# Kernel tuning notes

Measured on AMD Instinct MI355X. Metric: run time of the kernel, lower is better.

The kernel has to match this reference:

```python
import jax, jax.numpy as jnp
import numpy as np

# Blade order: 1 | e0 e1 e2 e3 | e01 e02 e03 e12 e13 e23 | e012 e013 e023 e123 | e0123
GRADE = jnp.array([0, 1, 1, 1, 1, 2, 2, 2, 2, 2, 2, 3, 3, 3, 3, 4])
# Invariant bilinear form <~A B>_0 for signature (+,-,-,-)
METRIC = jnp.array([1., 1., -1., -1., -1., -1., -1., -1., 1., 1., 1., 1., 1., 1., -1., -1.], dtype=jnp.float32)
NUM_HEADS, HID_MV, HID_S = 8, 8, 32


def equi_linear(mv, s, w_mv, w_s2mv, w_mv2s, w_s, b_mv, b_s):
    """Pin(1,3)-equivariant linear layer: grade-projection basis maps + scalar<->grade-0 mixing."""
    w16 = w_mv[:, :, GRADE]  # (out_mv, in_mv, 16): one weight per grade, broadcast over blades
    out_mv = jnp.einsum('oix,...ix->...ox', w16, mv)
    out_mv = out_mv.at[..., 0].add(jnp.einsum('oi,...i->...o', w_s2mv, s) + b_mv)
    out_s = (jnp.einsum('oi,...i->...o', w_s, s)
             + jnp.einsum('oi,...i->...o', w_mv2s, mv[..., 0]) + b_s)
    return out_mv, out_s


def setup_inputs() -> dict:
    key = jax.random.key(0)
    ks = jax.random.split(key, 20)
    B, Nq, Nkv = 4, 2048, 2048
    H, Cm, Cs = NUM_HEADS, HID_MV, HID_S

    def w(k, shape, fan_in):
        return jax.random.normal(k, shape, jnp.float32) / np.sqrt(fan_in).astype(np.float32)

    return {
        'multivectors_kv': jax.random.normal(ks[0], (B, Nkv, 16, 16), jnp.float32),
        'multivectors_q': jax.random.normal(ks[1], (B, Nq, 16, 16), jnp.float32),
        'scalars_kv': jax.random.normal(ks[2], (B, Nkv, 64), jnp.float32),
        'scalars_q': jax.random.normal(ks[3], (B, Nq, 64), jnp.float32),
        # q_linear: 16 mv -> Cm*H=64 mv, 64 s -> Cs*H=256 s
        'wq_mv': w(ks[4], (Cm * H, 16, 5), 16), 'wq_s2mv': w(ks[5], (Cm * H, 64), 64),
        'wq_mv2s': w(ks[6], (Cs * H, 16), 16), 'wq_s': w(ks[7], (Cs * H, 64), 64),
        'bq_mv': jnp.zeros((Cm * H,), jnp.float32), 'bq_s': jnp.zeros((Cs * H,), jnp.float32),
        # kv_linear: 16 mv -> 2*Cm=16 mv, 64 s -> 2*Cs=64 s (multi-query: shared across heads)
        'wkv_mv': w(ks[8], (2 * Cm, 16, 5), 16), 'wkv_s2mv': w(ks[9], (2 * Cm, 64), 64),
        'wkv_mv2s': w(ks[10], (2 * Cs, 16), 16), 'wkv_s': w(ks[11], (2 * Cs, 64), 64),
        'bkv_mv': jnp.zeros((2 * Cm,), jnp.float32), 'bkv_s': jnp.zeros((2 * Cs,), jnp.float32),
        # out_linear: Cm*H=64 mv -> 16 mv, Cs*H=256 s -> 64 s
        'wo_mv': w(ks[12], (16, Cm * H, 5), Cm * H), 'wo_s2mv': w(ks[13], (16, Cs * H), Cs * H),
        'wo_mv2s': w(ks[14], (64, Cm * H), Cm * H), 'wo_s': w(ks[15], (64, Cs * H), Cs * H),
        'bo_mv': jnp.zeros((16,), jnp.float32), 'bo_s': jnp.zeros((64,), jnp.float32),
        'head_scale': jnp.ones((H,), jnp.float32),
    }


def reference(multivectors_kv, multivectors_q, scalars_kv, scalars_q,
              wq_mv, wq_s2mv, wq_mv2s, wq_s, bq_mv, bq_s,
              wkv_mv, wkv_s2mv, wkv_mv2s, wkv_s, bkv_mv, bkv_s,
              wo_mv, wo_s2mv, wo_mv2s, wo_s, bo_mv, bo_s, head_scale):
    B, Nq = multivectors_q.shape[0], multivectors_q.shape[1]
    H, Cm, Cs = NUM_HEADS, HID_MV, HID_S

    q_mv, q_s = equi_linear(multivectors_q, scalars_q, wq_mv, wq_s2mv, wq_mv2s, wq_s, bq_mv, bq_s)
    kv_mv, kv_s = equi_linear(multivectors_kv, scalars_kv, wkv_mv, wkv_s2mv, wkv_mv2s, wkv_s, bkv_mv, bkv_s)
    k_mv, v_mv = jnp.split(kv_mv, 2, axis=-2)  # (B,Nkv,Cm,16) each
    k_s, v_s = jnp.split(kv_s, 2, axis=-1)     # (B,Nkv,Cs) each

    # einops '(hidden num_heads)': hidden is the outer factor
    q_mv = jnp.moveaxis(q_mv.reshape(B, Nq, Cm, H, 16), 3, 1)  # (B,H,Nq,Cm,16)
    q_s = jnp.moveaxis(q_s.reshape(B, Nq, Cs, H), 3, 1)        # (B,H,Nq,Cs)

    scale = np.float32(1.0 / np.sqrt(16 * Cm + Cs))  # flattened feature dim
    scores = (jnp.einsum('bhqcx,bkcx->bhqk', q_mv, k_mv * METRIC)
              + jnp.einsum('bhqs,bks->bhqk', q_s, k_s)) * scale
    attn = jax.nn.softmax(scores, axis=-1)  # (B,H,Nq,Nkv)
    h_mv = jnp.einsum('bhqk,bkcx->bhqcx', attn, v_mv)
    h_s = jnp.einsum('bhqk,bks->bhqs', attn, v_s)

    h_mv = h_mv * head_scale[None, :, None, None, None]
    h_s = h_s * head_scale[None, :, None, None]

    # '(n_heads hidden_channels)': heads outer
    h_mv = jnp.moveaxis(h_mv, 1, 2).reshape(B, Nq, H * Cm, 16)
    h_s = jnp.moveaxis(h_s, 1, 2).reshape(B, Nq, H * Cs)

    return equi_linear(h_mv, h_s, wo_mv, wo_s2mv, wo_mv2s, wo_s, bo_mv, bo_s)
```

## Files before the change

### kernel.cpp

```cpp
#include <hip/hip_runtime.h>
#include <hip/hip_bf16.h>
#include <cstdint>

#define H_  8
#define B_  4
#define NQ  2048
#define NKV 2048
#define DF  160

typedef __attribute__((ext_vector_type(8))) short bf16x8;
typedef __attribute__((ext_vector_type(4))) float f32x4;

__constant__ int   c_grade[16]  = {0,1,1,1,1,2,2,2,2,2,2,3,3,3,3,4};
__constant__ float c_metric[16] = {1.f,1.f,-1.f,-1.f,-1.f,-1.f,-1.f,-1.f,
                                   1.f,1.f,1.f,1.f,1.f,1.f,-1.f,-1.f};

#define SCALE_LOG2E 0.11405506f

__device__ __forceinline__ unsigned short f2bf(float f) {
    union { float f; unsigned u; } v; v.f = f;
    return (unsigned short)((v.u + 0x7FFFu + ((v.u >> 16) & 1u)) >> 16);
}
__device__ __forceinline__ float bf2f(unsigned short u) {
    union { unsigned u; float f; } v; v.u = ((unsigned)u) << 16;
    return v.f;
}

__global__ __launch_bounds__(256) void qproj_kernel(
    const float* __restrict__ mvq,
    const float* __restrict__ sq,
    const float* __restrict__ w_mv,
    const float* __restrict__ w_s2mv,
    const float* __restrict__ w_mv2s,
    const float* __restrict__ w_s,
    const float* __restrict__ b_mv,
    const float* __restrict__ b_s,
    unsigned short* __restrict__ Qbuf)
{
    const int tok0 = blockIdx.x * 16;
    const int b = tok0 / NQ, n0 = tok0 % NQ;
    const int t = threadIdx.x;

    __shared__ float mv_t[256][20];
    __shared__ float s_t[64][20];
    __shared__ float smadd[64][20];

    #pragma unroll
    for (int k = 0; k < 16; ++k)
        mv_t[t][k] = mvq[(size_t)(tok0 + k) * 256 + t];
    {
        int e = t & 63, tb = t >> 6;
        #pragma unroll
        for (int k = 0; k < 4; ++k)
            s_t[e][tb + 4 * k] = sq[(size_t)(tok0 + tb + 4 * k) * 64 + e];
    }
    __syncthreads();

    {
        int o = t >> 2, tg = t & 3;
        f32x4 acc = {0.f, 0.f, 0.f, 0.f};
        for (int i = 0; i < 64; ++i)
            acc += w_s2mv[o * 64 + i] * *(const f32x4*)&s_t[i][tg * 4];
        acc += b_mv[o];
        *(f32x4*)&smadd[o][tg * 4] = acc;
    }
    __syncthreads();

    const int x = t & 15;
    const int g = c_grade[x];
    const int obase = t >> 4;
    {
        float wreg[4][16];
        #pragma unroll
        for (int p = 0; p < 4; ++p) {
            int o = obase + 16 * p;
            #pragma unroll
            for (int i = 0; i < 16; ++i)
                wreg[p][i] = w_mv[(o * 16 + i) * 5 + g];
        }
        #pragma unroll
        for (int k = 0; k < 4; ++k) {
            f32x4 rows[16];
            #pragma unroll
            for (int i = 0; i < 16; ++i)
                rows[i] = *(const f32x4*)&mv_t[i * 16 + x][k * 4];
            #pragma unroll
            for (int p = 0; p < 4; ++p) {
                int o = obase + 16 * p;
                f32x4 acc = {0.f, 0.f, 0.f, 0.f};
                #pragma unroll
                for (int i = 0; i < 16; ++i)
                    acc += wreg[p][i] * rows[i];
                if (x == 0) acc += *(const f32x4*)&smadd[o][k * 4];
                int c = o >> 3, h = o & 7;
                #pragma unroll
                for (int j = 0; j < 4; ++j)
                    Qbuf[((size_t)(b * H_ + h) * NQ + n0 + k * 4 + j) * DF + c * 16 + x] =
                        f2bf(acc[j] * SCALE_LOG2E);
            }
        }
    }

    {
        f32x4 acc[4] = {{0,0,0,0},{0,0,0,0},{0,0,0,0},{0,0,0,0}};
        const float4* ws4 = (const float4*)w_s;
        #pragma unroll
        for (int ii = 0; ii < 16; ++ii) {
            float4 w4 = ws4[t * 16 + ii];
            #pragma unroll
            for (int c = 0; c < 4; ++c) {
                float w = (&w4.x)[c];
                #pragma unroll
                for (int k = 0; k < 4; ++k)
                    acc[k] += w * *(const f32x4*)&s_t[ii * 4 + c][k * 4];
            }
        }
        #pragma unroll
        for (int i = 0; i < 16; ++i) {
            float w = w_mv2s[t * 16 + i];
            #pragma unroll
            for (int k = 0; k < 4; ++k)
                acc[k] += w * *(const f32x4*)&mv_t[i * 16][k * 4];
        }
        float bs = b_s[t];
        int cs = t >> 3, h = t & 7;
        #pragma unroll
        for (int k = 0; k < 4; ++k)
            #pragma unroll
            for (int j = 0; j < 4; ++j)
                Qbuf[((size_t)(b * H_ + h) * NQ + n0 + k * 4 + j) * DF + 128 + cs] =
                    f2bf((acc[k][j] + bs) * SCALE_LOG2E);
    }
}

__global__ __launch_bounds__(256) void kvproj_kernel(
    const float* __restrict__ mvkv, const float* __restrict__ skv,
    const float* __restrict__ w_mv,
    const float* __restrict__ w_s2mv,
    const float* __restrict__ w_mv2s,
    const float* __restrict__ w_s,
    const float* __restrict__ b_mv,
    const float* __restrict__ b_s,
    unsigned short* __restrict__ Kbuf,
    unsigned short* __restrict__ Vtbuf)
{
    const int tok0 = blockIdx.x * 16;
    const int b = tok0 / NKV, n0 = tok0 % NKV;
    const int t = threadIdx.x;

    __shared__ float mv_t[256][20];
    __shared__ float s_t[64][20];
    __shared__ float smadd[16][20];

    #pragma unroll
    for (int k = 0; k < 16; ++k)
        mv_t[t][k] = mvkv[(size_t)(tok0 + k) * 256 + t];
    {
        int e = t & 63, tb = t >> 6;
        #pragma unroll
        for (int k = 0; k < 4; ++k)
            s_t[e][tb + 4 * k] = skv[(size_t)(tok0 + tb + 4 * k) * 64 + e];
    }
    __syncthreads();

    {
        int o = t >> 4, tau = t & 15;
        float acc = 0.f;
        for (int i = 0; i < 64; ++i)
            acc += w_s2mv[o * 64 + i] * s_t[i][tau];
        smadd[o][tau] = acc + b_mv[o];
    }
    __syncthreads();

    {
        int o = t >> 4, x = t & 15, g = c_grade[x];
        f32x4 acc[4] = {{0,0,0,0},{0,0,0,0},{0,0,0,0},{0,0,0,0}};
        #pragma unroll
        for (int i = 0; i < 16; ++i) {
            float w = w_mv[(o * 16 + i) * 5 + g];
            #pragma unroll
            for (int k = 0; k < 4; ++k)
                acc[k] += w * *(const f32x4*)&mv_t[i * 16 + x][k * 4];
        }
        if (x == 0) {
            #pragma unroll
            for (int k = 0; k < 4; ++k)
                acc[k] += *(const f32x4*)&smadd[o][k * 4];
        }
        if (o < 8) {
            float met = c_metric[x];
            #pragma unroll
            for (int k = 0; k < 4; ++k)
                #pragma unroll
                for (int j = 0; j < 4; ++j)
                    Kbuf[((size_t)b * NKV + n0 + k * 4 + j) * DF + o * 16 + x] =
                        f2bf(acc[k][j] * met);
        } else {
            uint4 pk[2];
            unsigned* pu = (unsigned*)&pk[0];
            #pragma unroll
            for (int q = 0; q < 8; ++q) {
                int k = q >> 1, j = (q & 1) * 2;
                pu[q] = (unsigned)f2bf(acc[k][j]) | ((unsigned)f2bf(acc[k][j + 1]) << 16);
            }
            unsigned short* dst = Vtbuf + ((size_t)b * DF + (o - 8) * 16 + x) * NKV + n0;
            ((uint4*)dst)[0] = pk[0];
            ((uint4*)dst)[1] = pk[1];
        }
    }

    {
        int o2 = t & 63, tg = t >> 6;
        f32x4 acc = {0.f, 0.f, 0.f, 0.f};
        const float4* ws4 = (const float4*)w_s;
        #pragma unroll
        for (int ii = 0; ii < 16; ++ii) {
            float4 w4 = ws4[o2 * 16 + ii];
            #pragma unroll
            for (int c = 0; c < 4; ++c)
                acc += (&w4.x)[c] * *(const f32x4*)&s_t[ii * 4 + c][tg * 4];
        }
        #pragma unroll
        for (int i = 0; i < 16; ++i)
            acc += w_mv2s[o2 * 16 + i] * *(const f32x4*)&mv_t[i * 16][tg * 4];
        acc += b_s[o2];
        if (o2 < 32) {
            #pragma unroll
            for (int j = 0; j < 4; ++j)
                Kbuf[((size_t)b * NKV + n0 + tg * 4 + j) * DF + 128 + o2] = f2bf(acc[j]);
        } else {
            uint2 pk;
            pk.x = (unsigned)f2bf(acc[0]) | ((unsigned)f2bf(acc[1]) << 16);
            pk.y = (unsigned)f2bf(acc[2]) | ((unsigned)f2bf(acc[3]) << 16);
            *(uint2*)(Vtbuf + ((size_t)b * DF + 128 + o2 - 32) * NKV + n0 + tg * 4) = pk;
        }
    }
}

__global__ __launch_bounds__(256, 2) void attn_kernel(
    const unsigned short* __restrict__ Qb,
    const unsigned short* __restrict__ Kb0,
    const unsigned short* __restrict__ Vb0,
    const float* __restrict__ head_scale,
    unsigned short* __restrict__ Hb)
{
    const int qt = blockIdx.x, hp = blockIdx.y, b = blockIdx.z;
    const int tid  = threadIdx.x;
    const int w    = tid >> 6;
    const int lane = tid & 63;
    const int l16  = lane & 15;
    const int lq   = lane >> 4;
    const int qbase = qt * 64;

    __shared__ __align__(16) unsigned short Ksh[64][168];
    __shared__ __align__(16) unsigned short Vsh[160][72];
    __shared__ __align__(16) unsigned short Psh[2][4][16][72];

    bf16x8 onesf;
    #pragma unroll
    for (int j = 0; j < 8; ++j) onesf[j] = (short)0x3F80;

    bf16x8 qf[2][5];
    #pragma unroll
    for (int s = 0; s < 2; ++s) {
        const unsigned short* qrow =
            Qb + ((size_t)(b * H_ + hp * 2 + s) * NQ + qbase + w * 16 + l16) * DF;
        #pragma unroll
        for (int ks = 0; ks < 5; ++ks)
            qf[s][ks] = *reinterpret_cast<const bf16x8*>(qrow + ks * 32 + lq * 8);
    }

    f32x4 O[2][11];
    #pragma unroll
    for (int s = 0; s < 2; ++s)
        #pragma unroll
        for (int d = 0; d < 11; ++d) O[s][d] = f32x4{0.f, 0.f, 0.f, 0.f};

    const unsigned short* Kb = Kb0 + (size_t)b * NKV * DF;
    const unsigned short* Vb = Vb0 + (size_t)b * DF * NKV;

    for (int kt = 0; kt < NKV / 64; ++kt) {
        __syncthreads();
        #pragma unroll
        for (int c = 0; c < 5; ++c) {
            int idx = tid + c * 256;
            int r = idx / 20, col = idx % 20;
            *reinterpret_cast<uint4*>(&Ksh[r][col * 8]) =
                *reinterpret_cast<const uint4*>(Kb + (size_t)(kt * 64 + r) * DF + col * 8);
        }
        #pragma unroll
        for (int c = 0; c < 5; ++c) {
            int idx = tid + c * 256;
            int r = idx >> 3, col = idx & 7;
            *reinterpret_cast<uint4*>(&Vsh[r][col * 8]) =
                *reinterpret_cast<const uint4*>(Vb + (size_t)r * NKV + kt * 64 + col * 8);
        }
        __syncthreads();

        f32x4 sc[2][4];
        #pragma unroll
        for (int nt = 0; nt < 4; ++nt) {
            sc[0][nt] = f32x4{0.f, 0.f, 0.f, 0.f};
            sc[1][nt] = f32x4{0.f, 0.f, 0.f, 0.f};
            #pragma unroll
            for (int ks = 0; ks < 5; ++ks) {
                bf16x8 kf = *reinterpret_cast<const bf16x8*>(
                    &Ksh[nt * 16 + l16][ks * 32 + lq * 8]);
                sc[0][nt] = __builtin_amdgcn_mfma_f32_16x16x32_bf16(qf[0][ks], kf, sc[0][nt], 0, 0, 0);
                sc[1][nt] = __builtin_amdgcn_mfma_f32_16x16x32_bf16(qf[1][ks], kf, sc[1][nt], 0, 0, 0);
            }
        }

        #pragma unroll
        for (int s = 0; s < 2; ++s)
            #pragma unroll
            for (int nt = 0; nt < 4; ++nt)
                #pragma unroll
                for (int r = 0; r < 4; ++r)
                    Psh[s][w][lq * 4 + r][nt * 16 + l16] =
                        f2bf(__builtin_amdgcn_exp2f(sc[s][nt][r]));

        #pragma unroll
        for (int k2 = 0; k2 < 2; ++k2) {
            bf16x8 pf0 = *reinterpret_cast<const bf16x8*>(&Psh[0][w][l16][k2 * 32 + lq * 8]);
            bf16x8 pf1 = *reinterpret_cast<const bf16x8*>(&Psh[1][w][l16][k2 * 32 + lq * 8]);
            O[0][10] = __builtin_amdgcn_mfma_f32_16x16x32_bf16(pf0, onesf, O[0][10], 0, 0, 0);
            O[1][10] = __builtin_amdgcn_mfma_f32_16x16x32_bf16(pf1, onesf, O[1][10], 0, 0, 0);
            #pragma unroll
            for (int d = 0; d < 10; ++d) {
                bf16x8 vf = *reinterpret_cast<const bf16x8*>(
                    &Vsh[d * 16 + l16][k2 * 32 + lq * 8]);
                O[0][d] = __builtin_amdgcn_mfma_f32_16x16x32_bf16(pf0, vf, O[0][d], 0, 0, 0);
                O[1][d] = __builtin_amdgcn_mfma_f32_16x16x32_bf16(pf1, vf, O[1][d], 0, 0, 0);
            }
        }
    }

    #pragma unroll
    for (int s = 0; s < 2; ++s) {
        float hsc = head_scale[hp * 2 + s];
        #pragma unroll
        for (int r = 0; r < 4; ++r) {
            float inv = hsc / O[s][10][r];
            int qrow = qbase + w * 16 + lq * 4 + r;
            unsigned short* orow =
                Hb + ((size_t)(b * H_ + hp * 2 + s) * NQ + qrow) * DF;
            #pragma unroll
            for (int d = 0; d < 10; ++d)
                orow[d * 16 + l16] = f2bf(O[s][d][r] * inv);
        }
    }
}

__global__ __launch_bounds__(256) void oproj_kernel(
    const unsigned short* __restrict__ Hb,
    const float* __restrict__ w_mv,
    const float* __restrict__ w_s2mv,
    const float* __restrict__ w_mv2s,
    const float* __restrict__ w_s,
    const float* __restrict__ b_mv,
    const float* __restrict__ b_s,
    float* __restrict__ out)
{
    const int tok0 = blockIdx.x * 8;
    const int b = tok0 / NQ, n0 = tok0 % NQ;
    const int t = threadIdx.x;

    __shared__ float hmv_t[1024][12];
    __shared__ float hs_t[256][12];
    __shared__ float s2v[16][8];

    #pragma unroll
    for (int hh = 0; hh < 8; ++hh) {
        #pragma unroll
        for (int j = 0; j < 5; ++j) {
            int flat = t + 256 * j;
            int tau = flat / 160, d = flat % 160;
            float v = bf2f(Hb[((size_t)(b * H_ + hh) * NQ + n0 + tau) * DF + d]);
            if (d < 128) hmv_t[hh * 128 + d][tau] = v;
            else         hs_t[hh * 32 + d - 128][tau] = v;
        }
    }
    __syncthreads();

    {
        int o2 = t >> 4, tau = (t >> 1) & 7, ih = t & 1;
        float acc = 0.f;
        for (int ii = 0; ii < 128; ++ii) {
            int i = ih * 128 + ii;
            acc += w_s2mv[o2 * 256 + i] * hs_t[i][tau];
        }
        acc += __shfl_xor(acc, 1);
        if (ih == 0) s2v[o2][tau] = acc + b_mv[o2];
    }
    __syncthreads();

    {
        int o2 = t >> 4, x = t & 15, g = c_grade[x];
        f32x4 a0 = {0,0,0,0}, a1 = {0,0,0,0};
        for (int i = 0; i < 64; ++i) {
            float w = w_mv[(o2 * 64 + i) * 5 + g];
            a0 += w * *(const f32x4*)&hmv_t[i * 16 + x][0];
            a1 += w * *(const f32x4*)&hmv_t[i * 16 + x][4];
        }
        if (x == 0) {
            a0 += *(const f32x4*)&s2v[o2][0];
            a1 += *(const f32x4*)&s2v[o2][4];
        }
        #pragma unroll
        for (int j = 0; j < 4; ++j) {
            out[(size_t)(tok0 + j) * 256 + o2 * 16 + x] = a0[j];
            out[(size_t)(tok0 + 4 + j) * 256 + o2 * 16 + x] = a1[j];
        }
    }

    {
        int o2 = t & 63, th = t >> 6;
        float a0 = b_s[o2], a1 = b_s[o2];
        const float4* ws4 = (const float4*)w_s;
        for (int ii = 0; ii < 64; ++ii) {
            float4 w4 = ws4[o2 * 64 + ii];
            #pragma unroll
            for (int c = 0; c < 4; ++c) {
                int i = ii * 4 + c;
                float w = (&w4.x)[c];
                a0 += w * hs_t[i][th * 2];
                a1 += w * hs_t[i][th * 2 + 1];
            }
        }
        for (int i = 0; i < 64; ++i) {
            float w = w_mv2s[o2 * 64 + i];
            a0 += w * hmv_t[i * 16][th * 2];
            a1 += w * hmv_t[i * 16][th * 2 + 1];
        }
        size_t sbase = (size_t)B_ * NQ * 256;
        out[sbase + (size_t)(tok0 + th * 2) * 64 + o2] = a0;
        out[sbase + (size_t)(tok0 + th * 2 + 1) * 64 + o2] = a1;
    }
}

extern "C" void kernel_launch(void* const* d_in, const int* in_sizes, int n_in,
                              void* d_out, int out_size, void* d_ws, size_t ws_size,
                              hipStream_t stream) {
    const float* mv_kv  = (const float*)d_in[0];
    const float* mv_q   = (const float*)d_in[1];
    const float* s_kv   = (const float*)d_in[2];
    const float* s_q    = (const float*)d_in[3];
    const float* wq_mv  = (const float*)d_in[4];
    const float* wq_s2mv= (const float*)d_in[5];
    const float* wq_mv2s= (const float*)d_in[6];
    const float* wq_s   = (const float*)d_in[7];
    const float* bq_mv  = (const float*)d_in[8];
    const float* bq_s   = (const float*)d_in[9];
    const float* wkv_mv = (const float*)d_in[10];
    const float* wkv_s2mv=(const float*)d_in[11];
    const float* wkv_mv2s=(const float*)d_in[12];
    const float* wkv_s  = (const float*)d_in[13];
    const float* bkv_mv = (const float*)d_in[14];
    const float* bkv_s  = (const float*)d_in[15];
    const float* wo_mv  = (const float*)d_in[16];
    const float* wo_s2mv= (const float*)d_in[17];
    const float* wo_mv2s= (const float*)d_in[18];
    const float* wo_s   = (const float*)d_in[19];
    const float* bo_mv  = (const float*)d_in[20];
    const float* bo_s   = (const float*)d_in[21];
    const float* head_scale = (const float*)d_in[22];

    char* ws = (char*)d_ws;
    unsigned short* Qbuf  = (unsigned short*)(ws);
    unsigned short* Kbuf  = (unsigned short*)(ws + 20971520);
    unsigned short* Vtbuf = (unsigned short*)(ws + 23592960);
    unsigned short* Hbuf  = (unsigned short*)(ws + 26214400);

    qproj_kernel<<<B_ * NQ / 16, 256, 0, stream>>>(
        mv_q, s_q, wq_mv, wq_s2mv, wq_mv2s, wq_s, bq_mv, bq_s, Qbuf);
    kvproj_kernel<<<B_ * NKV / 16, 256, 0, stream>>>(
        mv_kv, s_kv, wkv_mv, wkv_s2mv, wkv_mv2s, wkv_s, bkv_mv, bkv_s, Kbuf, Vtbuf);
    dim3 g3(NQ / 64, H_ / 2, B_);
    attn_kernel<<<g3, 256, 0, stream>>>(Qbuf, Kbuf, Vtbuf, head_scale, Hbuf);
    oproj_kernel<<<B_ * NQ / 8, 256, 0, stream>>>(
        Hbuf, wo_mv, wo_s2mv, wo_mv2s, wo_s, bo_mv, bo_s, (float*)d_out);
}
```

Measured before the change: 290.4 us.

## Recast equivariant projections as dense bf16 MFMA GEMMs with expanded weights

Replaces the scalar-FMA q/kv/out projection kernels with weight-expansion kernels, which build dense bf16 matrices folding in grade broadcast, scalar mixing, bias (via a constant-one input column), metric and softmax scale. These are then consumed by MFMA-based GEMM kernels. The aim is to move the projection arithmetic onto matrix cores and cut FP32 VALU work. The cost is three extra launches per call to expand the weights, many zero-padded FLOPs, and inputs rounded to bf16 before the projections.

Result: slower. 332.2 us (+14.4%).

```diff
diff --git a/kernel.cpp b/kernel.cpp
--- a/kernel.cpp
+++ b/kernel.cpp
@@ -21,218 +21,315 @@
     union { float f; unsigned u; } v; v.f = f;
     return (unsigned short)((v.u + 0x7FFFu + ((v.u >> 16) & 1u)) >> 16);
 }
-__device__ __forceinline__ float bf2f(unsigned short u) {
-    union { unsigned u; float f; } v; v.u = ((unsigned)u) << 16;
-    return v.f;
-}
-
-__global__ __launch_bounds__(256) void qproj_kernel(
-    const float* __restrict__ mvq,
-    const float* __restrict__ sq,
-    const float* __restrict__ w_mv,
-    const float* __restrict__ w_s2mv,
-    const float* __restrict__ w_mv2s,
-    const float* __restrict__ w_s,
-    const float* __restrict__ b_mv,
-    const float* __restrict__ b_s,
-    unsigned short* __restrict__ Qbuf)
-{
-    const int tok0 = blockIdx.x * 16;
+
+__global__ __launch_bounds__(256) void expand_wq(
+    const float* __restrict__ wmv, const float* __restrict__ ws2mv,
+    const float* __restrict__ wmv2s, const float* __restrict__ ws,
+    const float* __restrict__ bmv, const float* __restrict__ bs,
+    unsigned short* __restrict__ Wq)
+{
+    const int j = blockIdx.x;
+    const int h = j / 160, pos = j % 160;
+    for (int k = threadIdx.x; k < 352; k += 256) {
+        float val = 0.f;
+        if (pos < 128) {
+            int c = pos >> 4, x = pos & 15, o = c * 8 + h, g = c_grade[x];
+            if (k < 256)       { if ((k & 15) == x) val = wmv[(o*16 + (k>>4))*5 + g]; }
+            else if (k < 320)  { if (x == 0) val = ws2mv[o*64 + (k-256)]; }
+            else if (k == 320) { if (x == 0) val = bmv[o]; }
+        } else {
+            int cs = pos - 128, o2 = cs * 8 + h;
+            if (k < 256)       { if ((k & 15) == 0) val = wmv2s[o2*16 + (k>>4)]; }
+            else if (k < 320)  val = ws[o2*64 + (k-256)];
+            else if (k == 320) val = bs[o2];
+        }
+        Wq[(size_t)j*352 + k] = f2bf(val * SCALE_LOG2E);
+    }
+}
+
+__global__ __launch_bounds__(256) void expand_wkv(
+    const float* __restrict__ wmv, const float* __restrict__ ws2mv,
+    const float* __restrict__ wmv2s, const float* __restrict__ ws,
+    const float* __restrict__ bmv, const float* __restrict__ bs,
+    unsigned short* __restrict__ Wkv)
+{
+    const int j = blockIdx.x;
+    const int side = j / 160, pos = j % 160;
+    for (int k = threadIdx.x; k < 352; k += 256) {
+        float val = 0.f, mult = 1.f;
+        if (pos < 128) {
+            int c = pos >> 4, x = pos & 15, o = side * 8 + c, g = c_grade[x];
+            if (side == 0) mult = c_metric[x];
+            if (k < 256)       { if ((k & 15) == x) val = wmv[(o*16 + (k>>4))*5 + g]; }
+            else if (k < 320)  { if (x == 0) val = ws2mv[o*64 + (k-256)]; }
+            else if (k == 320) { if (x == 0) val = bmv[o]; }
+        } else {
+            int s = pos - 128, o2 = side * 32 + s;
+            if (k < 256)       { if ((k & 15) == 0) val = wmv2s[o2*16 + (k>>4)]; }
+            else if (k < 320)  val = ws[o2*64 + (k-256)];
+            else if (k == 320) val = bs[o2];
+        }
+        Wkv[(size_t)j*352 + k] = f2bf(val * mult);
+    }
+}
+
+__global__ __launch_bounds__(256) void expand_wo(
+    const float* __restrict__ wmv, const float* __restrict__ ws2mv,
+    const float* __restrict__ wmv2s, const float* __restrict__ ws,
+    const float* __restrict__ bmv, const float* __restrict__ bs,
+    unsigned short* __restrict__ Wo)
+{
+    const int j = blockIdx.x;
+    for (int k = threadIdx.x; k < 1408; k += 256) {
+        float val = 0.f;
+        if (j < 256) {
+            int o2 = j >> 4, x = j & 15, g = c_grade[x];
+            if (k < 1280) {
+                int hh = k / 160, pp = k % 160;
+                if (pp < 128) { if ((pp & 15) == x) val = wmv[(o2*64 + hh*8 + (pp>>4))*5 + g]; }
+                else          { if (x == 0) val = ws2mv[o2*256 + hh*32 + (pp-128)]; }
+            } else if (k == 1280) { if (x == 0) val = bmv[o2]; }
+        } else {
+            int o2 = j - 256;
+            if (k < 1280) {
+                int hh = k / 160, pp = k % 160;
+                if (pp < 128) { if ((pp & 15) == 0) val = wmv2s[o2*64 + hh*8 + (pp>>4)]; }
+                else          val = ws[o2*256 + hh*32 + (pp-128)];
+            } else if (k == 1280) val = bs[o2];
+        }
+        Wo[(size_t)j*1408 + k] = f2bf(val);
+    }
+}
+
+#define ASTR 360
+#define WSTR 40
+
+__global__ __launch_bounds__(256) void gemm_q(
+    const float* __restrict__ mvq, const float* __restrict__ sq,
+    const unsigned short* __restrict__ Wq, unsigned short* __restrict__ Qbuf)
+{
+    const int tok0 = blockIdx.x * 64, h = blockIdx.y;
     const int b = tok0 / NQ, n0 = tok0 % NQ;
-    const int t = threadIdx.x;
-
-    __shared__ float mv_t[256][20];
-    __shared__ float s_t[64][20];
-    __shared__ float smadd[64][20];
-
-    #pragma unroll
-    for (int k = 0; k < 16; ++k)
-        mv_t[t][k] = mvq[(size_t)(tok0 + k) * 256 + t];
-    {
-        int e = t & 63, tb = t >> 6;
-        #pragma unroll
-        for (int k = 0; k < 4; ++k)
-            s_t[e][tb + 4 * k] = sq[(size_t)(tok0 + tb + 4 * k) * 64 + e];
+    const int t = threadIdx.x, w = t >> 6, lane = t & 63, l16 = lane & 15, lq = lane >> 4;
+
+    __shared__ __align__(16) unsigned short Ash[64][ASTR];
+    __shared__ __align__(16) unsigned short Wsh[160][WSTR];
+
+    const float4* mv4 = (const float4*)(mvq + (size_t)tok0 * 256);
+    const float4* s4  = (const float4*)(sq  + (size_t)tok0 * 64);
+    #pragma unroll
+    for (int r = 0; r < 20; ++r) {
+        int slot = t + 256 * r;
+        int tok = slot / 80, q = slot % 80;
+        float4 v = (q < 64) ? mv4[tok * 64 + q] : s4[tok * 16 + (q - 64)];
+        int col = (q < 64) ? q * 4 : 256 + (q - 64) * 4;
+        unsigned lo = (unsigned)f2bf(v.x) | ((unsigned)f2bf(v.y) << 16);
+        unsigned hi = (unsigned)f2bf(v.z) | ((unsigned)f2bf(v.w) << 16);
+        uint2 u; u.x = lo; u.y = hi;
+        *(uint2*)&Ash[tok][col] = u;
+    }
+    #pragma unroll
+    for (int r = 0; r < 9; ++r) {
+        int idx = t + 256 * r;
+        int tok = idx / 36, cc = idx % 36;
+        Ash[tok][320 + cc] = (cc == 0) ? (unsigned short)0x3F80 : (unsigned short)0;
     }
     __syncthreads();
 
-    {
-        int o = t >> 2, tg = t & 3;
-        f32x4 acc = {0.f, 0.f, 0.f, 0.f};
-        for (int i = 0; i < 64; ++i)
-            acc += w_s2mv[o * 64 + i] * *(const f32x4*)&s_t[i][tg * 4];
-        acc += b_mv[o];
-        *(f32x4*)&smadd[o][tg * 4] = acc;
+    bf16x8 af[11];
+    #pragma unroll
+    for (int ks = 0; ks < 11; ++ks)
+        af[ks] = *(const bf16x8*)&Ash[w * 16 + l16][ks * 32 + lq * 8];
+
+    f32x4 acc[10];
+    #pragma unroll
+    for (int nt = 0; nt < 10; ++nt) acc[nt] = f32x4{0.f, 0.f, 0.f, 0.f};
+
+    const unsigned short* Wbase = Wq + (size_t)h * 160 * 352;
+    for (int ks = 0; ks < 11; ++ks) {
+        __syncthreads();
+        #pragma unroll
+        for (int r = 0; r < 3; ++r) {
+            int s = t + 256 * r;
+            if (s < 640) {
+                int row = s >> 2, c4 = s & 3;
+                *(uint4*)&Wsh[row][c4 * 8] =
+                    *(const uint4*)(Wbase + (size_t)row * 352 + ks * 32 + c4 * 8);
+            }
+        }
+        __syncthreads();
+        #pragma unroll
+        for (int nt = 0; nt < 10; ++nt) {
+            bf16x8 wf = *(const bf16x8*)&Wsh[nt * 16 + l16][lq * 8];
+            acc[nt] = __builtin_amdgcn_mfma_f32_16x16x32_bf16(af[ks], wf, acc[nt], 0, 0, 0);
+        }
+    }
+
+    unsigned short* qb = Qbuf + ((size_t)(b * H_ + h) * NQ + n0) * DF;
+    #pragma unroll
+    for (int nt = 0; nt < 10; ++nt)
+        #pragma unroll
+        for (int r = 0; r < 4; ++r) {
+            int tok = w * 16 + 4 * lq + r;
+            qb[(size_t)tok * DF + nt * 16 + l16] = f2bf(acc[nt][r]);
+        }
+}
+
+__global__ __launch_bounds__(256) void gemm_kv(
+    const float* __restrict__ mvkv, const float* __restrict__ skv,
+    const unsigned short* __restrict__ Wkv,
+    unsigned short* __restrict__ Kbuf, unsigned short* __restrict__ Vtbuf)
+{
+    const int tok0 = blockIdx.x * 64, slice = blockIdx.y;
+    const int b = tok0 / NKV, n0 = tok0 % NKV;
+    const int t = threadIdx.x, w = t >> 6, lane = t & 63, l16 = lane & 15, lq = lane >> 4;
+
+    __shared__ __align__(16) unsigned short Ash[64][ASTR];
+    __shared__ __align__(16) unsigned short Wsh[160][WSTR];
+
+    const float4* mv4 = (const float4*)(mvkv + (size_t)tok0 * 256);
+    const float4* s4  = (const float4*)(skv  + (size_t)tok0 * 64);
+    #pragma unroll
+    for (int r = 0; r < 20; ++r) {
+        int slot = t + 256 * r;
+        int tok = slot / 80, q = slot % 80;
+        float4 v = (q < 64) ? mv4[tok * 64 + q] : s4[tok * 16 + (q - 64)];
+        int col = (q < 64) ? q * 4 : 256 + (q - 64) * 4;
+        unsigned lo = (unsigned)f2bf(v.x) | ((unsigned)f2bf(v.y) << 16);
+        unsigned hi = (unsigned)f2bf(v.z) | ((unsigned)f2bf(v.w) << 16);
+        uint2 u; u.x = lo; u.y = hi;
+        *(uint2*)&Ash[tok][col] = u;
+    }
+    #pragma unroll
+    for (int r = 0; r < 9; ++r) {
+        int idx = t + 256 * r;
+        int tok = idx / 36, cc = idx % 36;
+        Ash[tok][320 + cc] = (cc == 0) ? (unsigned short)0x3F80 : (unsigned short)0;
     }
     __syncthreads();
 
-    const int x = t & 15;
-    const int g = c_grade[x];
-    const int obase = t >> 4;
-    {
-        float wreg[4][16];
-        #pragma unroll
-        for (int p = 0; p < 4; ++p) {
-            int o = obase + 16 * p;
-            #pragma unroll
-            for (int i = 0; i < 16; ++i)
-                wreg[p][i] = w_mv[(o * 16 + i) * 5 + g];
-        }
-        #pragma unroll
-        for (int k = 0; k < 4; ++k) {
-            f32x4 rows[16];
-            #pragma unroll
-            for (int i = 0; i < 16; ++i)
-                rows[i] = *(const f32x4*)&mv_t[i * 16 + x][k * 4];
-            #pragma unroll
-            for (int p = 0; p < 4; ++p) {
-                int o = obase + 16 * p;
-                f32x4 acc = {0.f, 0.f, 0.f, 0.f};
-                #pragma unroll
-                for (int i = 0; i < 16; ++i)
-                    acc += wreg[p][i] * rows[i];
-                if (x == 0) acc += *(const f32x4*)&smadd[o][k * 4];
-                int c = o >> 3, h = o & 7;
-                #pragma unroll
-                for (int j = 0; j < 4; ++j)
-                    Qbuf[((size_t)(b * H_ + h) * NQ + n0 + k * 4 + j) * DF + c * 16 + x] =
-                        f2bf(acc[j] * SCALE_LOG2E);
-            }
-        }
-    }
-
-    {
-        f32x4 acc[4] = {{0,0,0,0},{0,0,0,0},{0,0,0,0},{0,0,0,0}};
-        const float4* ws4 = (const float4*)w_s;
-        #pragma unroll
-        for (int ii = 0; ii < 16; ++ii) {
-            float4 w4 = ws4[t * 16 + ii];
-            #pragma unroll
-            for (int c = 0; c < 4; ++c) {
-                float w = (&w4.x)[c];
-                #pragma unroll
-                for (int k = 0; k < 4; ++k)
-                    acc[k] += w * *(const f32x4*)&s_t[ii * 4 + c][k * 4];
-            }
-        }
-        #pragma unroll
-        for (int i = 0; i < 16; ++i) {
-            float w = w_mv2s[t * 16 + i];
-            #pragma unroll
-            for (int k = 0; k < 4; ++k)
-                acc[k] += w * *(const f32x4*)&mv_t[i * 16][k * 4];
-        }
-        float bs = b_s[t];
-        int cs = t >> 3, h = t & 7;
-        #pragma unroll
-        for (int k = 0; k < 4; ++k)
-            #pragma unroll
-            for (int j = 0; j < 4; ++j)
-                Qbuf[((size_t)(b * H_ + h) * NQ + n0 + k * 4 + j) * DF + 128 + cs] =
-                    f2bf((acc[k][j] + bs) * SCALE_LOG2E);
-    }
-}
-
-__global__ __launch_bounds__(256) void kvproj_kernel(
-    const float* __restrict__ mvkv, const float* __restrict__ skv,
-    const float* __restrict__ w_mv,
-    const float* __restrict__ w_s2mv,
-    const float* __restrict__ w_mv2s,
-    const float* __restrict__ w_s,
-    const float* __restrict__ b_mv,
-    const float* __restrict__ b_s,
-    unsigned short* __restrict__ Kbuf,
-    unsigned short* __restrict__ Vtbuf)
-{
-    const int tok0 = blockIdx.x * 16;
-    const int b = tok0 / NKV, n0 = tok0 % NKV;
-    const int t = threadIdx.x;
-
-    __shared__ float mv_t[256][20];
-    __shared__ float s_t[64][20];
-    __shared__ float smadd[16][20];
-
-    #pragma unroll
-    for (int k = 0; k < 16; ++k)
-        mv_t[t][k] = mvkv[(size_t)(tok0 + k) * 256 + t];
-    {
-        int e = t & 63, tb = t >> 6;
-        #pragma unroll
-        for (int k = 0; k < 4; ++k)
-            s_t[e][tb + 4 * k] = skv[(size_t)(tok0 + tb + 4 * k) * 64 + e];
-    }
-    __syncthreads();
-
-    {
-        int o = t >> 4, tau = t & 15;
-        float acc = 0.f;
-        for (int i = 0; i < 64; ++i)
-            acc += w_s2mv[o * 64 + i] * s_t[i][tau];
-        smadd[o][tau] = acc + b_mv[o];
-    }
-    __syncthreads();
-
-    {
-        int o = t >> 4, x = t & 15, g = c_grade[x];
-        f32x4 acc[4] = {{0,0,0,0},{0,0,0,0},{0,0,0,0},{0,0,0,0}};
-        #pragma unroll
-        for (int i = 0; i < 16; ++i) {
-            float w = w_mv[(o * 16 + i) * 5 + g];
-            #pragma unroll
-            for (int k = 0; k < 4; ++k)
-                acc[k] += w * *(const f32x4*)&mv_t[i * 16 + x][k * 4];
-        }
-        if (x == 0) {
-            #pragma unroll
-            for (int k = 0; k < 4; ++k)
-                acc[k] += *(const f32x4*)&smadd[o][k * 4];
-        }
-        if (o < 8) {
-            float met = c_metric[x];
-            #pragma unroll
-            for (int k = 0; k < 4; ++k)
-                #pragma unroll
-                for (int j = 0; j < 4; ++j)
-                    Kbuf[((size_t)b * NKV + n0 + k * 4 + j) * DF + o * 16 + x] =
-                        f2bf(acc[k][j] * met);
-        } else {
-            uint4 pk[2];
-            unsigned* pu = (unsigned*)&pk[0];
-            #pragma unroll
-            for (int q = 0; q < 8; ++q) {
-                int k = q >> 1, j = (q & 1) * 2;
-                pu[q] = (unsigned)f2bf(acc[k][j]) | ((unsigned)f2bf(acc[k][j + 1]) << 16);
-            }
-            unsigned short* dst = Vtbuf + ((size_t)b * DF + (o - 8) * 16 + x) * NKV + n0;
-            ((uint4*)dst)[0] = pk[0];
-            ((uint4*)dst)[1] = pk[1];
-        }
-    }
-
-    {
-        int o2 = t & 63, tg = t >> 6;
-        f32x4 acc = {0.f, 0.f, 0.f, 0.f};
-        const float4* ws4 = (const float4*)w_s;
-        #pragma unroll
-        for (int ii = 0; ii < 16; ++ii) {
-            float4 w4 = ws4[o2 * 16 + ii];
-            #pragma unroll
-            for (int c = 0; c < 4; ++c)
-                acc += (&w4.x)[c] * *(const f32x4*)&s_t[ii * 4 + c][tg * 4];
-        }
-        #pragma unroll
-        for (int i = 0; i < 16; ++i)
-            acc += w_mv2s[o2 * 16 + i] * *(const f32x4*)&mv_t[i * 16][tg * 4];
-        acc += b_s[o2];
-        if (o2 < 32) {
-            #pragma unroll
-            for (int j = 0; j < 4; ++j)
-                Kbuf[((size_t)b * NKV + n0 + tg * 4 + j) * DF + 128 + o2] = f2bf(acc[j]);
-        } else {
-            uint2 pk;
-            pk.x = (unsigned)f2bf(acc[0]) | ((unsigned)f2bf(acc[1]) << 16);
-            pk.y = (unsigned)f2bf(acc[2]) | ((unsigned)f2bf(acc[3]) << 16);
-            *(uint2*)(Vtbuf + ((size_t)b * DF + 128 + o2 - 32) * NKV + n0 + tg * 4) = pk;
+    bf16x8 af[11];
+    #pragma unroll
+    for (int ks = 0; ks < 11; ++ks)
+        af[ks] = *(const bf16x8*)&Ash[w * 16 + l16][ks * 32 + lq * 8];
+
+    f32x4 acc[10];
+    #pragma unroll
+    for (int nt = 0; nt < 10; ++nt) acc[nt] = f32x4{0.f, 0.f, 0.f, 0.f};
+
+    const unsigned short* Wbase = Wkv + (size_t)slice * 160 * 352;
+    for (int ks = 0; ks < 11; ++ks) {
+        __syncthreads();
+        #pragma unroll
+        for (int r = 0; r < 3; ++r) {
+            int s = t + 256 * r;
+            if (s < 640) {
+                int row = s >> 2, c4 = s & 3;
+                *(uint4*)&Wsh[row][c4 * 8] =
+                    *(const uint4*)(Wbase + (size_t)row * 352 + ks * 32 + c4 * 8);
+            }
+        }
+        __syncthreads();
+        #pragma unroll
+        for (int nt = 0; nt < 10; ++nt) {
+            bf16x8 wf = *(const bf16x8*)&Wsh[nt * 16 + l16][lq * 8];
+            acc[nt] = __builtin_amdgcn_mfma_f32_16x16x32_bf16(af[ks], wf, acc[nt], 0, 0, 0);
+        }
+    }
+
+    if (slice == 0) {
+        unsigned short* kb = Kbuf + ((size_t)b * NKV + n0) * DF;
+        #pragma unroll
+        for (int nt = 0; nt < 10; ++nt)
+            #pragma unroll
+            for (int r = 0; r < 4; ++r) {
+                int tok = w * 16 + 4 * lq + r;
+                kb[(size_t)tok * DF + nt * 16 + l16] = f2bf(acc[nt][r]);
+            }
+    } else {
+        unsigned short* vb = Vtbuf + (size_t)b * DF * NKV;
+        #pragma unroll
+        for (int nt = 0; nt < 10; ++nt) {
+            int pos = nt * 16 + l16;
+            unsigned lo = (unsigned)f2bf(acc[nt][0]) | ((unsigned)f2bf(acc[nt][1]) << 16);
+            unsigned hi = (unsigned)f2bf(acc[nt][2]) | ((unsigned)f2bf(acc[nt][3]) << 16);
+            uint2 u; u.x = lo; u.y = hi;
+            *(uint2*)(vb + (size_t)pos * NKV + n0 + w * 16 + 4 * lq) = u;
+        }
+    }
+}
+
+__global__ __launch_bounds__(256) void gemm_o(
+    const unsigned short* __restrict__ Hb, const unsigned short* __restrict__ Wo,
+    float* __restrict__ out)
+{
+    const int tok0 = blockIdx.x * 64, slice = blockIdx.y;
+    const int b = tok0 / NQ, n0 = tok0 % NQ;
+    const int t = threadIdx.x, w = t >> 6, lane = t & 63, l16 = lane & 15, lq = lane >> 4;
+
+    __shared__ __align__(16) unsigned short Ash[64][ASTR];
+    __shared__ __align__(16) unsigned short Wsh[160][WSTR];
+
+    f32x4 acc[10];
+    #pragma unroll
+    for (int nt = 0; nt < 10; ++nt) acc[nt] = f32x4{0.f, 0.f, 0.f, 0.f};
+
+    const unsigned short* Wbase = Wo + (size_t)slice * 160 * 1408;
+
+    for (int kc = 0; kc < 4; ++kc) {
+        __syncthreads();
+        #pragma unroll
+        for (int r = 0; r < 11; ++r) {
+            int s = t + 256 * r;
+            int tok = s / 44, g = s % 44;
+            int f0 = kc * 352 + g * 8;
+            uint4 val;
+            if (f0 < 1280) {
+                int hh = f0 / 160, pp = f0 % 160;
+                val = *(const uint4*)(Hb + ((size_t)(b * H_ + hh) * NQ + n0 + tok) * DF + pp);
+            } else if (f0 == 1280) {
+                val.x = 0x3F80u; val.y = 0; val.z = 0; val.w = 0;
+            } else {
+                val.x = 0; val.y = 0; val.z = 0; val.w = 0;
+            }
+            *(uint4*)&Ash[tok][g * 8] = val;
+        }
+        __syncthreads();
+
+        bf16x8 af[11];
+        #pragma unroll
+        for (int ks = 0; ks < 11; ++ks)
+            af[ks] = *(const bf16x8*)&Ash[w * 16 + l16][ks * 32 + lq * 8];
+
+        for (int ks = 0; ks < 11; ++ks) {
+            __syncthreads();
+            #pragma unroll
+            for (int r = 0; r < 3; ++r) {
+                int s = t + 256 * r;
+                if (s < 640) {
+                    int row = s >> 2, c4 = s & 3;
+                    *(uint4*)&Wsh[row][c4 * 8] =
+                        *(const uint4*)(Wbase + (size_t)row * 1408 + kc * 352 + ks * 32 + c4 * 8);
+                }
+            }
+            __syncthreads();
+            #pragma unroll
+            for (int nt = 0; nt < 10; ++nt) {
+                bf16x8 wf = *(const bf16x8*)&Wsh[nt * 16 + l16][lq * 8];
+                acc[nt] = __builtin_amdgcn_mfma_f32_16x16x32_bf16(af[ks], wf, acc[nt], 0, 0, 0);
+            }
+        }
+    }
+
+    const size_t sbase = (size_t)B_ * NQ * 256;
+    #pragma unroll
+    for (int nt = 0; nt < 10; ++nt) {
+        int j = slice * 160 + nt * 16 + l16;
+        #pragma unroll
+        for (int r = 0; r < 4; ++r) {
+            size_t tok = tok0 + w * 16 + 4 * lq + r;
+            if (j < 256) out[tok * 256 + j] = acc[nt][r];
+            else         out[sbase + tok * 64 + (j - 256)] = acc[nt][r];
         }
     }
 }
@@ -349,93 +446,6 @@
             for (int d = 0; d < 10; ++d)
                 orow[d * 16 + l16] = f2bf(O[s][d][r] * inv);
         }
-    }
-}
-
-__global__ __launch_bounds__(256) void oproj_kernel(
-    const unsigned short* __restrict__ Hb,
-    const float* __restrict__ w_mv,
-    const float* __restrict__ w_s2mv,
-    const float* __restrict__ w_mv2s,
-    const float* __restrict__ w_s,
-    const float* __restrict__ b_mv,
-    const float* __restrict__ b_s,
-    float* __restrict__ out)
-{
-    const int tok0 = blockIdx.x * 8;
-    const int b = tok0 / NQ, n0 = tok0 % NQ;
-    const int t = threadIdx.x;
-
-    __shared__ float hmv_t[1024][12];
-    __shared__ float hs_t[256][12];
-    __shared__ float s2v[16][8];
-
-    #pragma unroll
-    for (int hh = 0; hh < 8; ++hh) {
-        #pragma unroll
-        for (int j = 0; j < 5; ++j) {
-            int flat = t + 256 * j;
-            int tau = flat / 160, d = flat % 160;
-            float v = bf2f(Hb[((size_t)(b * H_ + hh) * NQ + n0 + tau) * DF + d]);
-            if (d < 128) hmv_t[hh * 128 + d][tau] = v;
-            else         hs_t[hh * 32 + d - 128][tau] = v;
-        }
-    }
-    __syncthreads();
-
-    {
-        int o2 = t >> 4, tau = (t >> 1) & 7, ih = t & 1;
-        float acc = 0.f;
-        for (int ii = 0; ii < 128; ++ii) {
-            int i = ih * 128 + ii;
-            acc += w_s2mv[o2 * 256 + i] * hs_t[i][tau];
-        }
-        acc += __shfl_xor(acc, 1);
-        if (ih == 0) s2v[o2][tau] = acc + b_mv[o2];
-    }
-    __syncthreads();
-
-    {
-        int o2 = t >> 4, x = t & 15, g = c_grade[x];
-        f32x4 a0 = {0,0,0,0}, a1 = {0,0,0,0};
-        for (int i = 0; i < 64; ++i) {
-            float w = w_mv[(o2 * 64 + i) * 5 + g];
-            a0 += w * *(const f32x4*)&hmv_t[i * 16 + x][0];
-            a1 += w * *(const f32x4*)&hmv_t[i * 16 + x][4];
-        }
-        if (x == 0) {
-            a0 += *(const f32x4*)&s2v[o2][0];
-            a1 += *(const f32x4*)&s2v[o2][4];
-        }
-        #pragma unroll
-        for (int j = 0; j < 4; ++j) {
-            out[(size_t)(tok0 + j) * 256 + o2 * 16 + x] = a0[j];
-            out[(size_t)(tok0 + 4 + j) * 256 + o2 * 16 + x] = a1[j];
-        }
-    }
-
-    {
-        int o2 = t & 63, th = t >> 6;
-        float a0 = b_s[o2], a1 = b_s[o2];
-        const float4* ws4 = (const float4*)w_s;
-        for (int ii = 0; ii < 64; ++ii) {
-            float4 w4 = ws4[o2 * 64 + ii];
-            #pragma unroll
-            for (int c = 0; c < 4; ++c) {
-                int i = ii * 4 + c;
-                float w = (&w4.x)[c];
-                a0 += w * hs_t[i][th * 2];
-                a1 += w * hs_t[i][th * 2 + 1];
-            }
-        }
-        for (int i = 0; i < 64; ++i) {
-            float w = w_mv2s[o2 * 64 + i];
-            a0 += w * hmv_t[i * 16][th * 2];
-            a1 += w * hmv_t[i * 16][th * 2 + 1];
-        }
-        size_t sbase = (size_t)B_ * NQ * 256;
-        out[sbase + (size_t)(tok0 + th * 2) * 64 + o2] = a0;
-        out[sbase + (size_t)(tok0 + th * 2 + 1) * 64 + o2] = a1;
     }
 }
 
@@ -471,13 +481,19 @@
     unsigned short* Kbuf  = (unsigned short*)(ws + 20971520);
     unsigned short* Vtbuf = (unsigned short*)(ws + 23592960);
     unsigned short* Hbuf  = (unsigned short*)(ws + 26214400);
-
-    qproj_kernel<<<B_ * NQ / 16, 256, 0, stream>>>(
-        mv_q, s_q, wq_mv, wq_s2mv, wq_mv2s, wq_s, bq_mv, bq_s, Qbuf);
-    kvproj_kernel<<<B_ * NKV / 16, 256, 0, stream>>>(
-        mv_kv, s_kv, wkv_mv, wkv_s2mv, wkv_mv2s, wkv_s, bkv_mv, bkv_s, Kbuf, Vtbuf);
+    unsigned short* Wq    = (unsigned short*)(ws + 47185920);
+    unsigned short* Wkv   = (unsigned short*)(ws + 48087040);
+    unsigned short* Wo    = (unsigned short*)(ws + 48312320);
+
+    expand_wq <<<1280, 256, 0, stream>>>(wq_mv, wq_s2mv, wq_mv2s, wq_s, bq_mv, bq_s, Wq);
+    expand_wkv<<<320, 256, 0, stream>>>(wkv_mv, wkv_s2mv, wkv_mv2s, wkv_s, bkv_mv, bkv_s, Wkv);
+    expand_wo <<<320, 256, 0, stream>>>(wo_mv, wo_s2mv, wo_mv2s, wo_s, bo_mv, bo_s, Wo);
+
+    gemm_q <<<dim3(128, 8), 256, 0, stream>>>(mv_q, s_q, Wq, Qbuf);
+    gemm_kv<<<dim3(128, 2), 256, 0, stream>>>(mv_kv, s_kv, Wkv, Kbuf, Vtbuf);
+
     dim3 g3(NQ / 64, H_ / 2, B_);
     attn_kernel<<<g3, 256, 0, stream>>>(Qbuf, Kbuf, Vtbuf, head_scale, Hbuf);
-    oproj_kernel<<<B_ * NQ / 8, 256, 0, stream>>>(
-        Hbuf, wo_mv, wo_s2mv, wo_mv2s, wo_s, bo_mv, bo_s, (float*)d_out);
-}
+
+    gemm_o<<<dim3(128, 2), 256, 0, stream>>>(Hbuf, Wo, (float*)d_out);
+}
```
